# Kernel tuning notes

Hardware: AMD Instinct MI355X
Metric: run time of the kernel (lower is better)

## Reference

```python
import jax, jax.numpy as jnp
import numpy as np

SCALE = 16.0 / 8  # alpha / rank

def setup_inputs() -> dict:
    key = jax.random.key(0)
    k1, k2, k3, k4 = jax.random.split(key, 4)
    B, S, D_IN, D_OUT, R = 4, 2048, 4096, 4096, 8
    x = jax.random.normal(k1, (B, S, D_IN), dtype=jnp.float32)
    weight = jax.random.normal(k2, (D_OUT, D_IN), dtype=jnp.float32) * (1.0 / np.sqrt(D_IN))
    lora_A = jax.random.normal(k3, (R, D_IN), dtype=jnp.float32) * (1.0 / np.sqrt(D_IN))
    lora_B = jax.random.normal(k4, (D_OUT, R), dtype=jnp.float32) * 0.01
    return {"x": x, "weight": weight, "lora_A": lora_A, "lora_B": lora_B}

def reference(x, weight, lora_A, lora_B):
    # base: x @ W^T  -> [B, S, out]
    base_out = jnp.einsum('bsd,od->bso', x, weight)
    # low-rank path, chained as (x @ A^T) @ B^T (same math as x @ (B@A)^T)
    xa = jnp.einsum('bsd,rd->bsr', x, lora_A)      # [B, S, r]
    lora_out = jnp.einsum('bsr,or->bso', xa, lora_B)  # [B, S, out]
    return base_out + SCALE * lora_out
```

## Files before the change

### kernel.cpp

```cpp
#include <hip/hip_runtime.h>
#include <hip/hip_bf16.h>

typedef unsigned short u16;
typedef __attribute__((ext_vector_type(8))) __bf16 bf16x8;
typedef __attribute__((ext_vector_type(4))) float f32x4;
typedef __attribute__((ext_vector_type(8))) unsigned short ushort8;

#define GM 8192
#define GN 4096
#define GK 4096
#define NT (GK / 64)

__device__ __forceinline__ u16 f2bf(float f) {
  unsigned u = __float_as_uint(f);
  u += 0x7fffu + ((u >> 16) & 1u);
  return (u16)(u >> 16);
}

__global__ void build_weff(const float* __restrict__ W,
                           const float* __restrict__ lA,
                           const float* __restrict__ lB,
                           u16* __restrict__ Weff) {
  const int o = blockIdx.x;
  float b[8];
#pragma unroll
  for (int r = 0; r < 8; ++r) b[r] = 2.0f * lB[o * 8 + r];
  const float* wrow = W + (size_t)o * GK;
  u16* orow = Weff + (size_t)o * GK;
  for (int d = threadIdx.x * 4; d < GK; d += blockDim.x * 4) {
    float4 w = *reinterpret_cast<const float4*>(wrow + d);
    float a0 = w.x, a1 = w.y, a2 = w.z, a3 = w.w;
#pragma unroll
    for (int r = 0; r < 8; ++r) {
      float4 a = *reinterpret_cast<const float4*>(lA + r * GK + d);
      a0 += b[r] * a.x; a1 += b[r] * a.y; a2 += b[r] * a.z; a3 += b[r] * a.w;
    }
    ushort4 p;
    p.x = f2bf(a0); p.y = f2bf(a1); p.z = f2bf(a2); p.w = f2bf(a3);
    *reinterpret_cast<ushort4*>(orow + d) = p;
  }
}

__global__ void cvt_bf16(const float* __restrict__ x, u16* __restrict__ xb) {
  const size_t i = ((size_t)blockIdx.x * blockDim.x + threadIdx.x) * 8;
  float4 v0 = *reinterpret_cast<const float4*>(x + i);
  float4 v1 = *reinterpret_cast<const float4*>(x + i + 4);
  ushort8 o;
  o[0] = f2bf(v0.x); o[1] = f2bf(v0.y); o[2] = f2bf(v0.z); o[3] = f2bf(v0.w);
  o[4] = f2bf(v1.x); o[5] = f2bf(v1.y); o[6] = f2bf(v1.z); o[7] = f2bf(v1.w);
  *reinterpret_cast<ushort8*>(xb + i) = o;
}

__device__ __forceinline__ void gload16(const u16* g, u16* l) {
  __builtin_amdgcn_global_load_lds(
      (const __attribute__((address_space(1))) void*)g,
      (__attribute__((address_space(3))) void*)l, 16, 0, 0);
}

#define BAR()                                  \
  do {                                         \
    asm volatile("" ::: "memory");             \
    __builtin_amdgcn_s_barrier();              \
    asm volatile("" ::: "memory");             \
  } while (0)

__global__ __launch_bounds__(512, 2) void gemm256(const u16* __restrict__ Ab,
                                                  const u16* __restrict__ Bb,
                                                  float* __restrict__ C) {
  __shared__ u16 lds[2][2][256 * 64];

  const int tid = threadIdx.x;
  const int wv = tid >> 6;
  const int l = tid & 63;

  const int nwg = gridDim.x;
  const int cpx = nwg >> 3;
  const int wg = ((int)blockIdx.x & 7) * cpx + ((int)blockIdx.x >> 3);
  const int tm = wg >> 4;
  const int tn = wg & 15;

  const int wr = wv >> 2;
  const int wc = wv & 3;

  const int srow = (wv << 3) + (l >> 3);
  const int srl = ((wv & 1) << 3) | (l >> 3);
  const int skel = ((l & 7) << 3) ^ ((srl & 0xE) << 2);
  const u16* aG = Ab + (size_t)(tm * 256) * GK;
  const u16* bG = Bb + (size_t)(tn * 256) * GK;

  const int frow = l & 15;
  const int fksw = ((l >> 4) << 3) ^ ((frow & 0xE) << 2);
  const int arow = wr * 128 + frow;
  const int brow = wc * 64 + frow;

  auto STAGE = [&](int th, int r) {
    const int k0 = th << 6;
    const u16* src = (r < 2 ? aG : bG) +
                     (size_t)((r & 1) * 128 + srow) * GK + k0 + skel;
    u16* dst = &lds[th & 1][r >> 1][(r & 1) * 8192 + wv * 512];
#pragma unroll
    for (int j = 0; j < 2; ++j)
      gload16(src + (size_t)(j * 64) * GK, dst + j * 4096);
  };

  STAGE(0, 0); STAGE(0, 1); STAGE(0, 2); STAGE(0, 3);
  STAGE(1, 0); STAGE(1, 1);

  f32x4 acc[8][4] = {};
  bf16x8 af[4][2], bfr0[2][2], bfr1[2][2];

  asm volatile("s_waitcnt vmcnt(4)" ::: "memory");
  BAR();

  for (int t = 0; t < NT; ++t) {
    const u16* A = &lds[t & 1][0][0];
    const u16* B = &lds[t & 1][1][0];
#pragma unroll
    for (int q = 0; q < 4; ++q) {
      if (q == 0) {
#pragma unroll
        for (int n = 0; n < 2; ++n)
#pragma unroll
          for (int s = 0; s < 2; ++s)
            bfr0[n][s] = *reinterpret_cast<const bf16x8*>(
                B + (brow + n * 16) * 64 + (fksw ^ (s << 5)));
#pragma unroll
        for (int m = 0; m < 4; ++m)
#pragma unroll
          for (int s = 0; s < 2; ++s)
            af[m][s] = *reinterpret_cast<const bf16x8*>(
                A + (arow + m * 16) * 64 + (fksw ^ (s << 5)));
      } else if (q == 1) {
#pragma unroll
        for (int n = 0; n < 2; ++n)
#pragma unroll
          for (int s = 0; s < 2; ++s)
            bfr1[n][s] = *reinterpret_cast<const bf16x8*>(
                B + (brow + (n + 2) * 16) * 64 + (fksw ^ (s << 5)));
      } else if (q == 2) {
#pragma unroll
        for (int m = 0; m < 4; ++m)
#pragma unroll
          for (int s = 0; s < 2; ++s)
            af[m][s] = *reinterpret_cast<const bf16x8*>(
                A + (arow + (m + 4) * 16) * 64 + (fksw ^ (s << 5)));
      }
      if (q == 0) { if (t + 1 < NT) STAGE(t + 1, 2); }
      else if (q == 1) { if (t + 1 < NT) STAGE(t + 1, 3); }
      else if (q == 3) { if (t + 2 < NT) { STAGE(t + 2, 0); STAGE(t + 2, 1); } }

      BAR();
      __builtin_amdgcn_s_setprio(1);
      {
        const int mo = (q >= 2) ? 4 : 0;
        const int no = (q == 1 || q == 2) ? 2 : 0;
#pragma unroll
        for (int m = 0; m < 4; ++m)
#pragma unroll
          for (int n = 0; n < 2; ++n)
#pragma unroll
            for (int s = 0; s < 2; ++s)
              acc[mo + m][no + n] = __builtin_amdgcn_mfma_f32_16x16x32_bf16(
                  af[m][s], (no ? bfr1 : bfr0)[n][s], acc[mo + m][no + n],
                  0, 0, 0);
      }
      __builtin_amdgcn_s_setprio(0);
      if (q == 3) {
        if (t < NT - 2)
          asm volatile("s_waitcnt vmcnt(4)" ::: "memory");
        else if (t == NT - 2)
          asm volatile("s_waitcnt vmcnt(0)" ::: "memory");
      }
      BAR();
    }
  }

  const int orow = tm * 256 + wr * 128 + ((l >> 4) << 2);
  const int ocol = tn * 256 + wc * 64 + (l & 15);
#pragma unroll
  for (int m = 0; m < 8; ++m)
#pragma unroll
    for (int n = 0; n < 4; ++n) {
      float* cp = C + (size_t)(orow + m * 16) * GN + (ocol + n * 16);
#pragma unroll
      for (int j = 0; j < 4; ++j) cp[(size_t)j * GN] = acc[m][n][j];
    }
}

extern "C" void kernel_launch(void* const* d_in, const int* in_sizes, int n_in,
                              void* d_out, int out_size, void* d_ws, size_t ws_size,
                              hipStream_t stream) {
  const float* x  = (const float*)d_in[0];
  const float* W  = (const float*)d_in[1];
  const float* lA = (const float*)d_in[2];
  const float* lB = (const float*)d_in[3];
  float* out = (float*)d_out;

  u16* weff = (u16*)d_ws;
  u16* xb = (u16*)((char*)d_ws + (size_t)GN * GK * sizeof(u16));

  build_weff<<<GN, 256, 0, stream>>>(W, lA, lB, weff);
  cvt_bf16<<<(size_t)GM * GK / (256 * 8), 256, 0, stream>>>(x, xb);
  gemm256<<<(GM / 256) * (GN / 256), 512, 0, stream>>>(xb, weff, out);
}
```

Measured before the change: 309.7 us.

## Simplify GEMM main loop to single-barrier double-buffered tile pipeline

Replaces the four-phase per-tile schedule, which had staggered global-to-LDS prefetches two tiles ahead and a barrier around each quarter, with a simpler loop. Each iteration now waits for all outstanding loads, takes one barrier, issues the whole next tile's loads into the other buffer, and then runs the four MFMA quarters. Separate A-fragment registers for the low and high halves let the LDS reads and MFMAs be scheduled freely between quarters. This removes most barriers per tile. The cost is a shallower prefetch, since each tile's loads must fully land before the next iteration starts.

```diff
diff --git a/kernel.cpp b/kernel.cpp
--- a/kernel.cpp
+++ b/kernel.cpp
@@ -104,75 +104,88 @@
   };
 
   STAGE(0, 0); STAGE(0, 1); STAGE(0, 2); STAGE(0, 3);
-  STAGE(1, 0); STAGE(1, 1);
 
   f32x4 acc[8][4] = {};
-  bf16x8 af[4][2], bfr0[2][2], bfr1[2][2];
-
-  asm volatile("s_waitcnt vmcnt(4)" ::: "memory");
-  BAR();
+  bf16x8 af_lo[4][2], af_hi[4][2], bfr0[2][2], bfr1[2][2];
 
   for (int t = 0; t < NT; ++t) {
+    asm volatile("s_waitcnt vmcnt(0)" ::: "memory");
+    BAR();
+
     const u16* A = &lds[t & 1][0][0];
     const u16* B = &lds[t & 1][1][0];
-#pragma unroll
-    for (int q = 0; q < 4; ++q) {
-      if (q == 0) {
-#pragma unroll
-        for (int n = 0; n < 2; ++n)
-#pragma unroll
-          for (int s = 0; s < 2; ++s)
-            bfr0[n][s] = *reinterpret_cast<const bf16x8*>(
-                B + (brow + n * 16) * 64 + (fksw ^ (s << 5)));
-#pragma unroll
-        for (int m = 0; m < 4; ++m)
-#pragma unroll
-          for (int s = 0; s < 2; ++s)
-            af[m][s] = *reinterpret_cast<const bf16x8*>(
-                A + (arow + m * 16) * 64 + (fksw ^ (s << 5)));
-      } else if (q == 1) {
-#pragma unroll
-        for (int n = 0; n < 2; ++n)
-#pragma unroll
-          for (int s = 0; s < 2; ++s)
-            bfr1[n][s] = *reinterpret_cast<const bf16x8*>(
-                B + (brow + (n + 2) * 16) * 64 + (fksw ^ (s << 5)));
-      } else if (q == 2) {
-#pragma unroll
-        for (int m = 0; m < 4; ++m)
-#pragma unroll
-          for (int s = 0; s < 2; ++s)
-            af[m][s] = *reinterpret_cast<const bf16x8*>(
-                A + (arow + (m + 4) * 16) * 64 + (fksw ^ (s << 5)));
-      }
-      if (q == 0) { if (t + 1 < NT) STAGE(t + 1, 2); }
-      else if (q == 1) { if (t + 1 < NT) STAGE(t + 1, 3); }
-      else if (q == 3) { if (t + 2 < NT) { STAGE(t + 2, 0); STAGE(t + 2, 1); } }
-
-      BAR();
-      __builtin_amdgcn_s_setprio(1);
-      {
-        const int mo = (q >= 2) ? 4 : 0;
-        const int no = (q == 1 || q == 2) ? 2 : 0;
-#pragma unroll
-        for (int m = 0; m < 4; ++m)
-#pragma unroll
-          for (int n = 0; n < 2; ++n)
-#pragma unroll
-            for (int s = 0; s < 2; ++s)
-              acc[mo + m][no + n] = __builtin_amdgcn_mfma_f32_16x16x32_bf16(
-                  af[m][s], (no ? bfr1 : bfr0)[n][s], acc[mo + m][no + n],
-                  0, 0, 0);
-      }
-      __builtin_amdgcn_s_setprio(0);
-      if (q == 3) {
-        if (t < NT - 2)
-          asm volatile("s_waitcnt vmcnt(4)" ::: "memory");
-        else if (t == NT - 2)
-          asm volatile("s_waitcnt vmcnt(0)" ::: "memory");
-      }
-      BAR();
+
+    if (t + 1 < NT) {
+      STAGE(t + 1, 0); STAGE(t + 1, 1); STAGE(t + 1, 2); STAGE(t + 1, 3);
     }
+
+#pragma unroll
+    for (int n = 0; n < 2; ++n)
+#pragma unroll
+      for (int s = 0; s < 2; ++s)
+        bfr0[n][s] = *reinterpret_cast<const bf16x8*>(
+            B + (brow + n * 16) * 64 + (fksw ^ (s << 5)));
+#pragma unroll
+    for (int m = 0; m < 4; ++m)
+#pragma unroll
+      for (int s = 0; s < 2; ++s)
+        af_lo[m][s] = *reinterpret_cast<const bf16x8*>(
+            A + (arow + m * 16) * 64 + (fksw ^ (s << 5)));
+    __builtin_amdgcn_s_setprio(1);
+#pragma unroll
+    for (int m = 0; m < 4; ++m)
+#pragma unroll
+      for (int n = 0; n < 2; ++n)
+#pragma unroll
+        for (int s = 0; s < 2; ++s)
+          acc[m][n] = __builtin_amdgcn_mfma_f32_16x16x32_bf16(
+              af_lo[m][s], bfr0[n][s], acc[m][n], 0, 0, 0);
+    __builtin_amdgcn_s_setprio(0);
+
+#pragma unroll
+    for (int n = 0; n < 2; ++n)
+#pragma unroll
+      for (int s = 0; s < 2; ++s)
+        bfr1[n][s] = *reinterpret_cast<const bf16x8*>(
+            B + (brow + (n + 2) * 16) * 64 + (fksw ^ (s << 5)));
+    __builtin_amdgcn_s_setprio(1);
+#pragma unroll
+    for (int m = 0; m < 4; ++m)
+#pragma unroll
+      for (int n = 0; n < 2; ++n)
+#pragma unroll
+        for (int s = 0; s < 2; ++s)
+          acc[m][n + 2] = __builtin_amdgcn_mfma_f32_16x16x32_bf16(
+              af_lo[m][s], bfr1[n][s], acc[m][n + 2], 0, 0, 0);
+    __builtin_amdgcn_s_setprio(0);
+
+#pragma unroll
+    for (int m = 0; m < 4; ++m)
+#pragma unroll
+      for (int s = 0; s < 2; ++s)
+        af_hi[m][s] = *reinterpret_cast<const bf16x8*>(
+            A + (arow + (m + 4) * 16) * 64 + (fksw ^ (s << 5)));
+    __builtin_amdgcn_s_setprio(1);
+#pragma unroll
+    for (int m = 0; m < 4; ++m)
+#pragma unroll
+      for (int n = 0; n < 2; ++n)
+#pragma unroll
+        for (int s = 0; s < 2; ++s)
+          acc[m + 4][n + 2] = __builtin_amdgcn_mfma_f32_16x16x32_bf16(
+              af_hi[m][s], bfr1[n][s], acc[m + 4][n + 2], 0, 0, 0);
+    __builtin_amdgcn_s_setprio(0);
+
+    __builtin_amdgcn_s_setprio(1);
+#pragma unroll
+    for (int m = 0; m < 4; ++m)
+#pragma unroll
+      for (int n = 0; n < 2; ++n)
+#pragma unroll
+        for (int s = 0; s < 2; ++s)
+          acc[m + 4][n] = __builtin_amdgcn_mfma_f32_16x16x32_bf16(
+              af_hi[m][s], bfr0[n][s], acc[m + 4][n], 0, 0, 0);
+    __builtin_amdgcn_s_setprio(0);
   }
 
   const int orow = tm * 256 + wr * 128 + ((l >> 4) << 2);
```

Result: faster. 299.1 us (-3.4%).
